# Kernel tuning notes

Hardware: AMD Instinct MI355X
Metric: run time of the kernel (lower is better)

## Reference

```python
import jax, jax.numpy as jnp
import numpy as np


def setup_inputs() -> dict:
    N, E, F, H, C = 50000, 400000, 256, 256, 64
    key = jax.random.key(0)
    ks = jax.random.split(key, 6)
    s = 1.0 / np.sqrt(F)
    return {
        "x": jax.random.normal(ks[0], (N, F), dtype=jnp.float32),
        "edge_index": jax.random.randint(ks[1], (2, E), 0, N, dtype=jnp.int64),
        "W1": jax.random.normal(ks[2], (F, H), dtype=jnp.float32) * s,
        "b1": jnp.zeros((H,), dtype=jnp.float32),
        "W2": jax.random.normal(ks[3], (H, H), dtype=jnp.float32) * s,
        "b2": jnp.zeros((H,), dtype=jnp.float32),
        "Wh": jax.random.normal(ks[4], (H, C), dtype=jnp.float32) * s,
        "bh": jnp.zeros((C,), dtype=jnp.float32),
    }


def _gcn_layer(x, row, col, norm, W, b, n_nodes):
    # linear first (PyG GCNLayer: x = self.linear(x) before propagate)
    h = x @ W + b                      # [N, H]
    msg = norm[:, None] * h[row]       # x_j = x[source]; scale by sym norm
    return jax.ops.segment_sum(msg, col, num_segments=n_nodes)  # aggr='add' at target


def reference(x, edge_index, W1, b1, W2, b2, Wh, bh):
    N = x.shape[0]
    # add self loops
    loops = jnp.arange(N, dtype=edge_index.dtype)
    row = jnp.concatenate([edge_index[0], loops])  # source
    col = jnp.concatenate([edge_index[1], loops])  # target
    # degree via scatter_add of ones on row (as in source)
    deg = jax.ops.segment_sum(jnp.ones(row.shape[0], dtype=x.dtype), row, num_segments=N)
    deg_inv_sqrt = jnp.where(deg > 0, jax.lax.rsqrt(jnp.maximum(deg, 1.0)), 0.0)
    norm = deg_inv_sqrt[row] * deg_inv_sqrt[col]
    # two GCN layers with ReLU (dropout inactive in eval mode)
    h = jax.nn.relu(_gcn_layer(x, row, col, norm, W1, b1, N))
    h = jax.nn.relu(_gcn_layer(h, row, col, norm, W2, b2, N))
    # vertex task: no pooling, just head
    return h @ Wh + bh
```

## Files before the change

### kernel.cpp

```cpp
#include <hip/hip_runtime.h>
#include <hip/hip_bf16.h>

typedef __attribute__((ext_vector_type(8))) short short8;
typedef __attribute__((ext_vector_type(4))) float f32x4;

static inline int cdiv(int a, int b) { return (a + b - 1) / b; }

__device__ inline float bf2f(unsigned short u) {
    union { unsigned int u; float f; } a; a.u = ((unsigned int)u) << 16; return a.f;
}
__device__ inline unsigned short f2bf(float f) {
    union { float f; unsigned int u; } a; a.f = f;
    unsigned int r = a.u + 0x7fff + ((a.u >> 16) & 1);
    return (unsigned short)(r >> 16);
}
__device__ inline void gload_lds16(const void* g, void* l) {
    __builtin_amdgcn_global_load_lds(
        (const __attribute__((address_space(1))) unsigned int*)g,
        (__attribute__((address_space(3))) unsigned int*)l, 16, 0, 0);
}

__global__ __launch_bounds__(256) void count_both_k(
    const int* __restrict__ rows, const int* __restrict__ cols,
    float* deg, int* indeg, int E)
{
    int e = blockIdx.x * 256 + threadIdx.x;
    if (e < E) {
        atomicAdd(&deg[rows[e]], 1.0f);
        atomicAdd(&indeg[cols[e]], 1);
    }
}

__global__ __launch_bounds__(256) void scan_block_k(
    const int* __restrict__ indeg, int* __restrict__ rowstart, int* __restrict__ bsums, int N)
{
    __shared__ int smem[256];
    int b = blockIdx.x, t = threadIdx.x;
    int base = b * 1024 + t * 4;
    int v0 = (base + 0 < N) ? indeg[base + 0] : 0;
    int v1 = (base + 1 < N) ? indeg[base + 1] : 0;
    int v2 = (base + 2 < N) ? indeg[base + 2] : 0;
    int v3 = (base + 3 < N) ? indeg[base + 3] : 0;
    int s = v0 + v1 + v2 + v3;
    smem[t] = s;
    __syncthreads();
    for (int off = 1; off < 256; off <<= 1) {
        int x = smem[t];
        int y = (t >= off) ? smem[t - off] : 0;
        __syncthreads();
        smem[t] = x + y;
        __syncthreads();
    }
    int excl = smem[t] - s;
    if (base + 0 < N) rowstart[base + 0] = excl;
    if (base + 1 < N) rowstart[base + 1] = excl + v0;
    if (base + 2 < N) rowstart[base + 2] = excl + v0 + v1;
    if (base + 3 < N) rowstart[base + 3] = excl + v0 + v1 + v2;
    if (t == 255) bsums[b] = smem[255];
}

__global__ __launch_bounds__(256) void scan_sums_k(int* bsums, int nb, int* rowstart, int N, int E) {
    __shared__ int smem[256];
    int t = threadIdx.x;
    int v = (t < nb) ? bsums[t] : 0;
    smem[t] = v;
    __syncthreads();
    for (int off = 1; off < 256; off <<= 1) {
        int x = smem[t];
        int y = (t >= off) ? smem[t - off] : 0;
        __syncthreads();
        smem[t] = x + y;
        __syncthreads();
    }
    if (t < nb) bsums[t] = smem[t] - v;
    if (t == 0) rowstart[N] = E;
}

__global__ __launch_bounds__(256) void scan_add_dinv_k(
    int* rowstart, int* cursor, const int* __restrict__ bsums, float* deg, int N)
{
    int i = blockIdx.x * 256 + threadIdx.x;
    if (i < N) {
        int v = rowstart[i] + bsums[i >> 10];
        rowstart[i] = v;
        cursor[i] = v;
        deg[i] = rsqrtf(deg[i] + 1.0f);
    }
}

__global__ __launch_bounds__(256) void fill_csr_k(
    const int* __restrict__ rows, const int* __restrict__ cols,
    int* cursor, int* __restrict__ csr, int E)
{
    int e = blockIdx.x * 256 + threadIdx.x;
    if (e < E) {
        int pos = atomicAdd(&cursor[cols[e]], 1);
        csr[pos] = rows[e];
    }
}

__global__ __launch_bounds__(256) void prep_weights_zero_k(
    const float* __restrict__ W1, const float* __restrict__ W2, const float* __restrict__ Wh,
    unsigned short* __restrict__ Wt1, unsigned short* __restrict__ Wt2, unsigned short* __restrict__ Wht,
    float4* __restrict__ zp, int nz4)
{
    int idx = blockIdx.x * 256 + threadIdx.x;
    if (idx < nz4) zp[idx] = make_float4(0.f, 0.f, 0.f, 0.f);
    if (idx < 65536) {
        int k = idx >> 8, m = idx & 255;
        Wt1[m * 256 + k] = f2bf(W1[idx]);
    } else if (idx < 131072) {
        int i = idx - 65536;
        int k = i >> 8, m = i & 255;
        Wt2[m * 256 + k] = f2bf(W2[i]);
    } else if (idx < 147456) {
        int i = idx - 131072;
        int k = i >> 6, m = i & 63;
        Wht[m * 256 + k] = f2bf(Wh[i]);
    }
}

template<int BN, int MODE, int ASRC>
__global__ __launch_bounds__(256) void gemm_mfma_k(
    const void* __restrict__ Asrc, const unsigned short* __restrict__ Wt,
    const float* __restrict__ bias, const float* __restrict__ rowscale,
    void* __restrict__ Cout, int N, int K, int Ncols)
{
    constexpr int NF = BN / 32;
    __shared__ __align__(16) unsigned short As[2][128 * 64];
    __shared__ __align__(16) unsigned short Bs[2][BN * 64];

    const unsigned short* Ab = (const unsigned short*)Asrc;
    const float* Af = (const float*)Asrc;

    const int tid = threadIdx.x;
    const int wid = tid >> 6;
    const int lane = tid & 63;
    const int wr = wid >> 1;
    const int wc = wid & 1;
    const int rowBase = blockIdx.x * 128;
    const int colBase = blockIdx.y * BN;

    f32x4 acc[4][NF];
    #pragma unroll
    for (int m = 0; m < 4; ++m)
        #pragma unroll
        for (int n = 0; n < NF; ++n)
            acc[m][n] = (f32x4)0.0f;

    const int sslot = (lane & 7) ^ (lane >> 3);

    float4 areg[4][2];

    auto stageA_g = [&](int buf, int k0) {
        #pragma unroll
        for (int it = 0; it < 4; ++it) {
            int ch = wid * 4 + it;
            int r = ch * 8 + (lane >> 3);
            int grow = rowBase + r; if (grow >= N) grow = N - 1;
            gload_lds16(Ab + (size_t)grow * K + k0 + sslot * 8, (void*)&As[buf][ch * 512]);
        }
    };
    auto issueA = [&](int k0) {
        #pragma unroll
        for (int it = 0; it < 4; ++it) {
            int ch = wid * 4 + it;
            int r = ch * 8 + (lane >> 3);
            int grow = rowBase + r; if (grow >= N) grow = N - 1;
            const float* src = Af + (size_t)grow * K + k0 + sslot * 8;
            areg[it][0] = *(const float4*)src;
            areg[it][1] = *(const float4*)(src + 4);
        }
    };
    auto writeA = [&](int buf) {
        #pragma unroll
        for (int it = 0; it < 4; ++it) {
            int ch = wid * 4 + it;
            short8 w;
            w[0] = (short)f2bf(areg[it][0].x); w[1] = (short)f2bf(areg[it][0].y);
            w[2] = (short)f2bf(areg[it][0].z); w[3] = (short)f2bf(areg[it][0].w);
            w[4] = (short)f2bf(areg[it][1].x); w[5] = (short)f2bf(areg[it][1].y);
            w[6] = (short)f2bf(areg[it][1].z); w[7] = (short)f2bf(areg[it][1].w);
            *(short8*)&As[buf][ch * 512 + lane * 8] = w;
        }
    };
    auto stageB = [&](int buf, int k0) {
        #pragma unroll
        for (int it = 0; it < NF; ++it) {
            int ch = wid * NF + it;
            int c = ch * 8 + (lane >> 3);
            gload_lds16(Wt + (size_t)(colBase + c) * K + k0 + sslot * 8, (void*)&Bs[buf][ch * 512]);
        }
    };

    const int nt = K >> 6;
    if constexpr (ASRC == 0) {
        stageA_g(0, 0);
        stageB(0, 0);
    } else {
        issueA(0);
        stageB(0, 0);
        writeA(0);
    }
    __syncthreads();

    int cur = 0;
    for (int t = 0; t < nt; ++t) {
        if (t + 1 < nt) {
            if constexpr (ASRC == 0) stageA_g(cur ^ 1, (t + 1) * 64);
            else issueA((t + 1) * 64);
            stageB(cur ^ 1, (t + 1) * 64);
        }
        #pragma unroll
        for (int ks = 0; ks < 2; ++ks) {
            short8 af[4];
            #pragma unroll
            for (int m = 0; m < 4; ++m) {
                int R = wr * 64 + m * 16 + (lane & 15);
                int p = (ks * 4 + (lane >> 4)) ^ (R & 7);
                af[m] = *(const short8*)(&As[cur][R * 64 + p * 8]);
            }
            #pragma unroll
            for (int n = 0; n < NF; ++n) {
                int Cc = wc * (BN / 2) + n * 16 + (lane & 15);
                int p = (ks * 4 + (lane >> 4)) ^ (Cc & 7);
                short8 bf = *(const short8*)(&Bs[cur][Cc * 64 + p * 8]);
                #pragma unroll
                for (int m = 0; m < 4; ++m)
                    acc[m][n] = __builtin_amdgcn_mfma_f32_16x16x32_bf16(af[m], bf, acc[m][n], 0, 0, 0);
            }
        }
        if (t + 1 < nt) {
            if constexpr (ASRC == 1) writeA(cur ^ 1);
            __syncthreads();
        }
        cur ^= 1;
    }

    float bv[NF];
    int colv[NF];
    #pragma unroll
    for (int n = 0; n < NF; ++n) {
        colv[n] = colBase + wc * (BN / 2) + n * 16 + (lane & 15);
        bv[n] = bias[colv[n]];
    }
    #pragma unroll
    for (int m = 0; m < 4; ++m) {
        #pragma unroll
        for (int q = 0; q < 4; ++q) {
            int row = rowBase + wr * 64 + m * 16 + (lane >> 4) * 4 + q;
            if (row >= N) continue;
            if (MODE == 0) {
                float sc = rowscale[row];
                unsigned short* Cb = (unsigned short*)Cout;
                #pragma unroll
                for (int n = 0; n < NF; ++n)
                    Cb[(size_t)row * Ncols + colv[n]] = f2bf((acc[m][n][q] + bv[n]) * sc);
            } else {
                float* Cf = (float*)Cout;
                #pragma unroll
                for (int n = 0; n < NF; ++n)
                    Cf[(size_t)row * Ncols + colv[n]] = acc[m][n][q] + bv[n];
            }
        }
    }
}

__global__ __launch_bounds__(256) void gather_agg_k(
    const int* __restrict__ rowstart, const int* __restrict__ csr,
    const float* __restrict__ dinv, const unsigned short* __restrict__ hp,
    unsigned short* __restrict__ out, int N)
{
    int c = __builtin_amdgcn_readfirstlane(blockIdx.x * 4 + (threadIdx.x >> 6));
    if (c >= N) return;
    int lane = threadIdx.x & 63;
    const ushort4* base = (const ushort4*)hp;
    int beg = rowstart[c], end = rowstart[c + 1];

    ushort4 sv = base[(size_t)c * 64 + lane];
    float a0 = bf2f(sv.x), a1 = bf2f(sv.y), a2 = bf2f(sv.z), a3 = bf2f(sv.w);

    int e = beg;
    for (; e + 8 <= end; e += 8) {
        ushort4 v0 = base[(size_t)csr[e + 0] * 64 + lane];
        ushort4 v1 = base[(size_t)csr[e + 1] * 64 + lane];
        ushort4 v2 = base[(size_t)csr[e + 2] * 64 + lane];
        ushort4 v3 = base[(size_t)csr[e + 3] * 64 + lane];
        ushort4 v4 = base[(size_t)csr[e + 4] * 64 + lane];
        ushort4 v5 = base[(size_t)csr[e + 5] * 64 + lane];
        ushort4 v6 = base[(size_t)csr[e + 6] * 64 + lane];
        ushort4 v7 = base[(size_t)csr[e + 7] * 64 + lane];
        a0 += bf2f(v0.x) + bf2f(v1.x) + bf2f(v2.x) + bf2f(v3.x)
            + bf2f(v4.x) + bf2f(v5.x) + bf2f(v6.x) + bf2f(v7.x);
        a1 += bf2f(v0.y) + bf2f(v1.y) + bf2f(v2.y) + bf2f(v3.y)
            + bf2f(v4.y) + bf2f(v5.y) + bf2f(v6.y) + bf2f(v7.y);
        a2 += bf2f(v0.z) + bf2f(v1.z) + bf2f(v2.z) + bf2f(v3.z)
            + bf2f(v4.z) + bf2f(v5.z) + bf2f(v6.z) + bf2f(v7.z);
        a3 += bf2f(v0.w) + bf2f(v1.w) + bf2f(v2.w) + bf2f(v3.w)
            + bf2f(v4.w) + bf2f(v5.w) + bf2f(v6.w) + bf2f(v7.w);
    }
    for (; e + 4 <= end; e += 4) {
        ushort4 v0 = base[(size_t)csr[e + 0] * 64 + lane];
        ushort4 v1 = base[(size_t)csr[e + 1] * 64 + lane];
        ushort4 v2 = base[(size_t)csr[e + 2] * 64 + lane];
        ushort4 v3 = base[(size_t)csr[e + 3] * 64 + lane];
        a0 += bf2f(v0.x) + bf2f(v1.x) + bf2f(v2.x) + bf2f(v3.x);
        a1 += bf2f(v0.y) + bf2f(v1.y) + bf2f(v2.y) + bf2f(v3.y);
        a2 += bf2f(v0.z) + bf2f(v1.z) + bf2f(v2.z) + bf2f(v3.z);
        a3 += bf2f(v0.w) + bf2f(v1.w) + bf2f(v2.w) + bf2f(v3.w);
    }
    for (; e < end; ++e) {
        ushort4 v0 = base[(size_t)csr[e] * 64 + lane];
        a0 += bf2f(v0.x); a1 += bf2f(v0.y); a2 += bf2f(v0.z); a3 += bf2f(v0.w);
    }

    float sc = dinv[c];
    ushort4 o;
    o.x = f2bf(fmaxf(sc * a0, 0.f));
    o.y = f2bf(fmaxf(sc * a1, 0.f));
    o.z = f2bf(fmaxf(sc * a2, 0.f));
    o.w = f2bf(fmaxf(sc * a3, 0.f));
    ((ushort4*)out)[(size_t)c * 64 + lane] = o;
}

extern "C" void kernel_launch(void* const* d_in, const int* in_sizes, int n_in,
                              void* d_out, int out_size, void* d_ws, size_t ws_size,
                              hipStream_t stream) {
    const float* x  = (const float*)d_in[0];
    const int*  ei  = (const int*)d_in[1];
    const float* W1 = (const float*)d_in[2];
    const float* b1 = (const float*)d_in[3];
    const float* W2 = (const float*)d_in[4];
    const float* b2 = (const float*)d_in[5];
    const float* Wh = (const float*)d_in[6];
    const float* bh = (const float*)d_in[7];
    float* out = (float*)d_out;

    const int N = in_sizes[0] / 256;
    const int E = in_sizes[1] / 2;
    const int H = 256;
    const int C = 64;
    const int* rows = ei;
    const int* cols = ei + E;

    char* ws = (char*)d_ws;
    size_t off = 0;
    auto alloc = [&](size_t bytes) {
        void* p = ws + off;
        off = (off + bytes + 255) & ~(size_t)255;
        return p;
    };
    float* deg      = (float*)alloc((size_t)2 * N * 4);
    int*   indeg    = (int*)(deg + N);
    int*   rowstart = (int*)alloc((size_t)(N + 1) * 4);
    int*   bsums    = (int*)alloc(256 * 4);
    int*   csr      = (int*)alloc((size_t)E * 4);
    unsigned short* bufH = (unsigned short*)alloc((size_t)N * H * 2);
    unsigned short* bufA = (unsigned short*)alloc((size_t)N * H * 2);
    unsigned short* Wt1  = (unsigned short*)alloc((size_t)H * H * 2);
    unsigned short* Wt2  = (unsigned short*)alloc((size_t)H * H * 2);
    unsigned short* Wht  = (unsigned short*)alloc((size_t)C * H * 2);

    const int nb = cdiv(N, 1024);

    prep_weights_zero_k<<<cdiv(147456, 256), 256, 0, stream>>>(
        W1, W2, Wh, Wt1, Wt2, Wht, (float4*)deg, 2 * N / 4);
    count_both_k<<<cdiv(E, 256), 256, 0, stream>>>(rows, cols, deg, indeg, E);
    scan_block_k<<<nb, 256, 0, stream>>>(indeg, rowstart, bsums, N);
    scan_sums_k<<<1, 256, 0, stream>>>(bsums, nb, rowstart, N, E);
    scan_add_dinv_k<<<cdiv(N, 256), 256, 0, stream>>>(rowstart, indeg, bsums, deg, N);
    fill_csr_k<<<cdiv(E, 256), 256, 0, stream>>>(rows, cols, indeg, csr, E);
    float* dinv = deg;

    dim3 g1(cdiv(N, 128), H / 128);
    dim3 gh(cdiv(N, 128), 1);

    gemm_mfma_k<128, 0, 1><<<g1, 256, 0, stream>>>(x, Wt1, b1, dinv, bufH, N, H, H);
    gather_agg_k<<<cdiv(N, 4), 256, 0, stream>>>(rowstart, csr, dinv, bufH, bufA, N);

    gemm_mfma_k<128, 0, 0><<<g1, 256, 0, stream>>>(bufA, Wt2, b2, dinv, bufH, N, H, H);
    gather_agg_k<<<cdiv(N, 4), 256, 0, stream>>>(rowstart, csr, dinv, bufH, bufA, N);

    gemm_mfma_k<64, 1, 0><<<gh, 256, 0, stream>>>(bufA, Wht, bh, nullptr, out, N, H, C);
}
```

Before: 206.1 us.

## Remap GEMM blocks so column-tile pairs share an XCD and fuse scan kernels

The two 256-column GEMMs now use a 1D grid in which consecutive dispatch slots are remapped so that both column tiles of a row block land on the same XCD (blockIdx mod 8). Both tiles then read the same A rows through one L2. The single-block scan_sums kernel is folded into scan_add_dinv: every block rescans the small block-sum array in shared memory, which removes one launch. The cost is redundant per-block scan work and some early-returning padding blocks.

```diff
diff --git a/kernel.cpp b/kernel.cpp
--- a/kernel.cpp
+++ b/kernel.cpp
@@ -59,33 +59,36 @@
     if (t == 255) bsums[b] = smem[255];
 }
 
-__global__ __launch_bounds__(256) void scan_sums_k(int* bsums, int nb, int* rowstart, int N, int E) {
-    __shared__ int smem[256];
+__global__ __launch_bounds__(256) void scan_add_dinv_k(
+    int* rowstart, int* cursor, const int* __restrict__ bsums, int nb,
+    float* deg, int N, int E)
+{
+    __shared__ int sb[64];
     int t = threadIdx.x;
-    int v = (t < nb) ? bsums[t] : 0;
-    smem[t] = v;
+    int v = 0;
+    if (t < 64) {
+        v = (t < nb) ? bsums[t] : 0;
+        sb[t] = v;
+    }
     __syncthreads();
-    for (int off = 1; off < 256; off <<= 1) {
-        int x = smem[t];
-        int y = (t >= off) ? smem[t - off] : 0;
+    for (int off = 1; off < 64; off <<= 1) {
+        int x = 0, y = 0;
+        if (t < 64) { x = sb[t]; y = (t >= off) ? sb[t - off] : 0; }
         __syncthreads();
-        smem[t] = x + y;
+        if (t < 64) sb[t] = x + y;
         __syncthreads();
     }
-    if (t < nb) bsums[t] = smem[t] - v;
-    if (t == 0) rowstart[N] = E;
-}
-
-__global__ __launch_bounds__(256) void scan_add_dinv_k(
-    int* rowstart, int* cursor, const int* __restrict__ bsums, float* deg, int N)
-{
-    int i = blockIdx.x * 256 + threadIdx.x;
+    if (t < 64) sb[t] -= v;
+    __syncthreads();
+
+    int i = blockIdx.x * 256 + t;
     if (i < N) {
-        int v = rowstart[i] + bsums[i >> 10];
-        rowstart[i] = v;
-        cursor[i] = v;
+        int r = rowstart[i] + sb[i >> 10];
+        rowstart[i] = r;
+        cursor[i] = r;
         deg[i] = rsqrtf(deg[i] + 1.0f);
     }
+    if (blockIdx.x == 0 && t == 0) rowstart[N] = E;
 }
 
 __global__ __launch_bounds__(256) void fill_csr_k(
@@ -120,7 +123,7 @@
     }
 }
 
-template<int BN, int MODE, int ASRC>
+template<int BN, int MODE, int ASRC, int NYB>
 __global__ __launch_bounds__(256) void gemm_mfma_k(
     const void* __restrict__ Asrc, const unsigned short* __restrict__ Wt,
     const float* __restrict__ bias, const float* __restrict__ rowscale,
@@ -132,14 +135,26 @@
 
     const unsigned short* Ab = (const unsigned short*)Asrc;
     const float* Af = (const float*)Asrc;
+
+    int bx, by;
+    if constexpr (NYB == 2) {
+        const int nXB = (N + 127) >> 7;
+        int d = blockIdx.x;
+        int xcd = d & 7, slot = d >> 3;
+        by = slot & 1;
+        bx = xcd + 8 * (slot >> 1);
+        if (bx >= nXB) return;
+    } else {
+        bx = blockIdx.x; by = 0;
+    }
 
     const int tid = threadIdx.x;
     const int wid = tid >> 6;
     const int lane = tid & 63;
     const int wr = wid >> 1;
     const int wc = wid & 1;
-    const int rowBase = blockIdx.x * 128;
-    const int colBase = blockIdx.y * BN;
+    const int rowBase = bx * 128;
+    const int colBase = by * BN;
 
     f32x4 acc[4][NF];
     #pragma unroll
@@ -367,19 +382,19 @@
         W1, W2, Wh, Wt1, Wt2, Wht, (float4*)deg, 2 * N / 4);
     count_both_k<<<cdiv(E, 256), 256, 0, stream>>>(rows, cols, deg, indeg, E);
     scan_block_k<<<nb, 256, 0, stream>>>(indeg, rowstart, bsums, N);
-    scan_sums_k<<<1, 256, 0, stream>>>(bsums, nb, rowstart, N, E);
-    scan_add_dinv_k<<<cdiv(N, 256), 256, 0, stream>>>(rowstart, indeg, bsums, deg, N);
+    scan_add_dinv_k<<<cdiv(N, 256), 256, 0, stream>>>(rowstart, indeg, bsums, nb, deg, N, E);
     fill_csr_k<<<cdiv(E, 256), 256, 0, stream>>>(rows, cols, indeg, csr, E);
     float* dinv = deg;
 
-    dim3 g1(cdiv(N, 128), H / 128);
-    dim3 gh(cdiv(N, 128), 1);
-
-    gemm_mfma_k<128, 0, 1><<<g1, 256, 0, stream>>>(x, Wt1, b1, dinv, bufH, N, H, H);
+    const int nXB = cdiv(N, 128);
+    dim3 g1(16 * cdiv(nXB, 8));
+    dim3 gh(nXB);
+
+    gemm_mfma_k<128, 0, 1, 2><<<g1, 256, 0, stream>>>(x, Wt1, b1, dinv, bufH, N, H, H);
     gather_agg_k<<<cdiv(N, 4), 256, 0, stream>>>(rowstart, csr, dinv, bufH, bufA, N);
 
-    gemm_mfma_k<128, 0, 0><<<g1, 256, 0, stream>>>(bufA, Wt2, b2, dinv, bufH, N, H, H);
+    gemm_mfma_k<128, 0, 0, 2><<<g1, 256, 0, stream>>>(bufA, Wt2, b2, dinv, bufH, N, H, H);
     gather_agg_k<<<cdiv(N, 4), 256, 0, stream>>>(rowstart, csr, dinv, bufH, bufA, N);
 
-    gemm_mfma_k<64, 1, 0><<<gh, 256, 0, stream>>>(bufA, Wht, bh, nullptr, out, N, H, C);
-}
+    gemm_mfma_k<64, 1, 0, 1><<<gh, 256, 0, stream>>>(bufA, Wht, bh, nullptr, out, N, H, C);
+}
```

New measurement: 198.9 us. -3.5%, faster.
